# Performance work log

Measured on AMD Instinct MI355X. Metric: run time of the kernel, lower is better.

Reference implementation:

```python
import jax, jax.numpy as jnp
import numpy as np

B, D, N, M, R, C = 512, 16, 64, 32, 32, 10  # batch, divisions, feat_in, feat_map, TR-rank, categories


def setup_inputs() -> dict:
    key = jax.random.key(0)
    k1, k2, k3, k4 = jax.random.split(key, 4)
    tensor = jax.random.normal(k1, (B, D, N), dtype=jnp.float32)
    W_fm = jax.random.normal(k2, (N, M), dtype=jnp.float32) / np.sqrt(N)
    b_fm = jax.random.normal(k3, (M,), dtype=jnp.float32) * 0.01
    # one [R, M, R] tensor-ring core per (category, division)
    G = jax.random.normal(k4, (C, D, R, M, R), dtype=jnp.float32) / np.sqrt(M * R)
    return {"tensor": tensor, "W_fm": W_fm, "b_fm": b_fm, "G": G}


def reference(tensor, W_fm, b_fm, G):
    # FeatureMap: learned linear n -> m applied per division  [B, D, M]
    feat = jnp.einsum('bdn,nm->bdm', tensor, W_fm) + b_fm
    # CoreKernelTensorRing per (category, division): [B,M] x [R,M,R] -> [B,R,R]
    cores = jnp.einsum('bdm,cdimj->cdbij', feat, G)  # [C, D, B, R, R]
    # __foward_products: chained batched matmul along divisions (structural loop, D fixed)
    prod = cores[:, 0]  # [C, B, R, R]
    for d in range(1, D):
        prod = jnp.matmul(prod, cores[:, d])
    # __calculate_traces: per-sample trace, one logit per category
    logits = jnp.einsum('cbii->bc', prod)  # [B, C]
    return jax.nn.log_softmax(logits, axis=1)
```

## Files before the change

### kernel.cpp

```cpp
#include <hip/hip_runtime.h>
#include <math.h>

#define BB 512
#define DD 16
#define NN 64
#define MM 32
#define RR 32
#define CC 10
#define BBLK 8
#define ROWH 40
#define BREGH 1304

typedef _Float16 v8h __attribute__((ext_vector_type(8)));
typedef float v4f __attribute__((ext_vector_type(4)));

union H8 { unsigned int u[4]; v8h h; _Float16 e[8]; };
union H4 { unsigned int u[2]; _Float16 e[4]; };

__global__ __launch_bounds__(256) void produce_kernel(
    const float* __restrict__ tensor, const float* __restrict__ W,
    const float* __restrict__ bias,   const float* __restrict__ G,
    _Float16* __restrict__ fh,        _Float16* __restrict__ gh) {
    __shared__ __align__(16) char smem[36864];
    const int t = threadIdx.x;
    if (blockIdx.x < 1024) {
        float* ten_s = (float*)smem;
        float* W_s   = (float*)smem + 512;
        const int bd0 = blockIdx.x * 8;
        if (t < 128)
            *(float4*)(ten_s + t * 4) = *(const float4*)(tensor + bd0 * NN + t * 4);
        *(float4*)(W_s + t * 4)        = *(const float4*)(W + t * 4);
        *(float4*)(W_s + 1024 + t * 4) = *(const float4*)(W + 1024 + t * 4);
        __syncthreads();
        const int m = t & 31, bd_l = t >> 5;
        float acc = bias[m];
#pragma unroll
        for (int n = 0; n < NN; ++n) acc += ten_s[bd_l * NN + n] * W_s[n * MM + m];
        fh[(bd0 + bd_l) * MM + m] = (_Float16)acc;
    } else {
        _Float16* lg = (_Float16*)smem;
        const int pb = blockIdx.x - 1024;
        const int c  = pb >> 5;
        const int d  = (pb >> 1) & 15;
        const int hf = pb & 1;
        const float* src = G + (size_t)(c * DD + d) * 32768 + hf * 16384;
#pragma unroll
        for (int k = 0; k < 16; ++k) {
            const int f = (k * 256 + t) * 4;
            float4 v = *(const float4*)(src + f);
            const int di = f >> 10, m = (f >> 5) & 31, j = f & 31;
            H4 hv;
            hv.e[0] = (_Float16)v.x; hv.e[1] = (_Float16)v.y;
            hv.e[2] = (_Float16)v.z; hv.e[3] = (_Float16)v.w;
            *(uint2*)(lg + di * 1152 + m * 36 + j) = make_uint2(hv.u[0], hv.u[1]);
        }
        __syncthreads();
#pragma unroll
        for (int k = 0; k < 8; ++k) {
            const int idx = k * 256 + t;
            const int tl = idx >> 6, ln = idx & 63;
            const int di = tl >> 1;
            const int q = ln >> 4, j4 = ln & 15;
            const int j = (tl & 1) * 16 + j4;
            H8 o;
#pragma unroll
            for (int r = 0; r < 8; ++r)
                o.e[r] = lg[di * 1152 + (8 * q + r) * 36 + j];
            const size_t gi = ((size_t)(c * DD + d) * 64 + hf * 32 + tl) * 64 + ln;
            *(v8h*)(gh + gi * 8) = o.h;
        }
    }
}

__global__ __launch_bounds__(512, 4) void chain_kernel(
    const _Float16* __restrict__ feat_h,
    const _Float16* __restrict__ g_h,
    float* __restrict__ logits)
{
    __shared__ __align__(16) _Float16 lds[BBLK * BREGH];

    const int bid = blockIdx.x;
    const int xcd = bid & 7;
    const int idx = bid >> 3;
    int c, sub;
    if (idx < 64) { c = xcd; sub = idx; }
    else {
        const int e = idx - 64;
        if (xcd < 4) { c = 8; sub = xcd * 16 + e; }
        else         { c = 9; sub = (xcd - 4) * 16 + e; }
    }
    const int b0 = sub * BBLK;

    const int t    = threadIdx.x;
    const int w    = t >> 6;
    const int lane = t & 63;
    const int q    = lane >> 4;
    const int j4   = lane & 15;

    const size_t gbase_c = (size_t)c * DD * 32768;
    const int bA = b0 + (j4 & 7);

    v8h afh = *(const v8h*)(feat_h + (size_t)bA * (DD * MM) + q * 8);
    v8h gf[8];
#pragma unroll
    for (int u = 0; u < 8; ++u)
        gf[u] = *(const v8h*)(g_h + gbase_c + ((size_t)(w * 8 + u) * 64 + lane) * 8);

    v8h pah[2];
    v4f acc[2][2];

    for (int d = 0; d < DD; ++d) {
        __syncthreads();
        v4f av[8];
#pragma unroll
        for (int u = 0; u < 8; ++u) {
            v4f z = {0.f, 0.f, 0.f, 0.f};
            av[u] = __builtin_amdgcn_mfma_f32_16x16x32_f16(afh, gf[u], z, 0, 0, 0);
        }
        if (d < DD - 1) {
            afh = *(const v8h*)(feat_h + (size_t)bA * (DD * MM) + (d + 1) * MM + q * 8);
            const size_t gb = gbase_c + (size_t)(d + 1) * 32768;
#pragma unroll
            for (int u = 0; u < 8; ++u)
                gf[u] = *(const v8h*)(g_h + gb + ((size_t)(w * 8 + u) * 64 + lane) * 8);
        }
        if (q < 2) {
#pragma unroll
            for (int jh = 0; jh < 2; ++jh)
#pragma unroll
                for (int reg = 0; reg < 4; ++reg) {
                    H4 hv;
                    hv.e[0] = (_Float16)av[0 + jh][reg];
                    hv.e[1] = (_Float16)av[2 + jh][reg];
                    hv.e[2] = (_Float16)av[4 + jh][reg];
                    hv.e[3] = (_Float16)av[6 + jh][reg];
                    *reinterpret_cast<uint2*>(
                        &lds[(4 * q + reg) * BREGH + (16 * jh + j4) * ROWH + 4 * w]) =
                        make_uint2(hv.u[0], hv.u[1]);
                }
        }
        __syncthreads();
        _Float16* base = lds + w * BREGH;
        if (d == 0) {
#pragma unroll
            for (int mi = 0; mi < 2; ++mi) {
                H8 a;
#pragma unroll
                for (int r = 0; r < 8; ++r)
                    a.e[r] = base[(8 * q + r) * ROWH + 16 * mi + j4];
                pah[mi] = a.h;
            }
        } else {
            v8h bf[2];
#pragma unroll
            for (int ni = 0; ni < 2; ++ni)
                bf[ni] = *(const v8h*)(base + (16 * ni + j4) * ROWH + 8 * q);
#pragma unroll
            for (int mi = 0; mi < 2; ++mi)
#pragma unroll
                for (int ni = 0; ni < 2; ++ni) {
                    v4f z = {0.f, 0.f, 0.f, 0.f};
                    acc[mi][ni] = __builtin_amdgcn_mfma_f32_16x16x32_f16(
                        pah[mi], bf[ni], z, 0, 0, 0);
                }
            if (d < DD - 1) {
#pragma unroll
                for (int mi = 0; mi < 2; ++mi)
#pragma unroll
                    for (int ni = 0; ni < 2; ++ni)
#pragma unroll
                        for (int reg = 0; reg < 4; ++reg)
                            base[(16 * mi + 4 * q + reg) * ROWH + 16 * ni + j4] =
                                (_Float16)acc[mi][ni][reg];
                __builtin_amdgcn_sched_barrier(0);
#pragma unroll
                for (int mi = 0; mi < 2; ++mi)
                    pah[mi] = *(const v8h*)(base + (16 * mi + j4) * ROWH + 8 * q);
            }
        }
    }

    float tr = 0.f;
    if (q == (j4 >> 2)) {
        int reg = j4 & 3;
        tr = acc[0][0][reg] + acc[1][1][reg];
    }
#pragma unroll
    for (int off = 32; off > 0; off >>= 1) tr += __shfl_down(tr, off);
    if (lane == 0) logits[(b0 + w) * CC + c] = tr;
}

__global__ void lsm_kernel(const float* __restrict__ logits,
                           float* __restrict__ out) {
    int b = blockIdx.x * blockDim.x + threadIdx.x;
    if (b >= BB) return;
    float x[CC];
    float mx = -1e30f;
#pragma unroll
    for (int c = 0; c < CC; ++c) { x[c] = logits[b * CC + c]; mx = fmaxf(mx, x[c]); }
    float s = 0.f;
#pragma unroll
    for (int c = 0; c < CC; ++c) s += expf(x[c] - mx);
    float ls = logf(s);
#pragma unroll
    for (int c = 0; c < CC; ++c) out[b * CC + c] = x[c] - mx - ls;
}

extern "C" void kernel_launch(void* const* d_in, const int* in_sizes, int n_in,
                              void* d_out, int out_size, void* d_ws, size_t ws_size,
                              hipStream_t stream) {
    const float* tensor = (const float*)d_in[0];
    const float* W      = (const float*)d_in[1];
    const float* bias   = (const float*)d_in[2];
    const float* G      = (const float*)d_in[3];
    float* out = (float*)d_out;

    const size_t FEAT = (size_t)BB * DD * MM;
    const size_t GPK  = (size_t)CC * DD * 64 * 64 * 8;
    _Float16* fh = (_Float16*)d_ws;
    _Float16* gh = fh + FEAT;
    float* logits = (float*)(gh + GPK);

    produce_kernel<<<1024 + 320, 256, 0, stream>>>(tensor, W, bias, G, fh, gh);
    chain_kernel<<<CC * (BB / BBLK), 512, 0, stream>>>(fh, gh, logits);
    lsm_kernel<<<(BB + 255) / 256, 256, 0, stream>>>(logits, out);
}
```

Before: 124.1 us.

## Halve chain_kernel block to 4 waves, each handling two samples and two tile groups

The chain kernel now launches 256 threads (4 waves) per block instead of 512. Each wave computes two groups of 8 G tiles in the core-construction stage and then runs the serial chain matmul for two batch samples instead of one. The G prefetch for the next division is removed, so G loads now happen inside the loop just before use. This cuts per-block thread count and barrier participants, but it drops the load/compute overlap and doubles the serial per-wave work, so latency per division may grow.

```diff
diff --git a/kernel.cpp b/kernel.cpp
--- a/kernel.cpp
+++ b/kernel.cpp
@@ -72,7 +72,7 @@
     }
 }
 
-__global__ __launch_bounds__(512, 4) void chain_kernel(
+__global__ __launch_bounds__(256, 4) void chain_kernel(
     const _Float16* __restrict__ feat_h,
     const _Float16* __restrict__ g_h,
     float* __restrict__ logits)
@@ -100,94 +100,106 @@
     const size_t gbase_c = (size_t)c * DD * 32768;
     const int bA = b0 + (j4 & 7);
 
-    v8h afh = *(const v8h*)(feat_h + (size_t)bA * (DD * MM) + q * 8);
-    v8h gf[8];
-#pragma unroll
-    for (int u = 0; u < 8; ++u)
-        gf[u] = *(const v8h*)(g_h + gbase_c + ((size_t)(w * 8 + u) * 64 + lane) * 8);
-
-    v8h pah[2];
-    v4f acc[2][2];
+    v8h pah[2][2];
+    v4f acc[2][2][2];
 
     for (int d = 0; d < DD; ++d) {
         __syncthreads();
-        v4f av[8];
-#pragma unroll
-        for (int u = 0; u < 8; ++u) {
-            v4f z = {0.f, 0.f, 0.f, 0.f};
-            av[u] = __builtin_amdgcn_mfma_f32_16x16x32_f16(afh, gf[u], z, 0, 0, 0);
-        }
-        if (d < DD - 1) {
-            afh = *(const v8h*)(feat_h + (size_t)bA * (DD * MM) + (d + 1) * MM + q * 8);
-            const size_t gb = gbase_c + (size_t)(d + 1) * 32768;
-#pragma unroll
-            for (int u = 0; u < 8; ++u)
-                gf[u] = *(const v8h*)(g_h + gb + ((size_t)(w * 8 + u) * 64 + lane) * 8);
-        }
-        if (q < 2) {
-#pragma unroll
-            for (int jh = 0; jh < 2; ++jh)
-#pragma unroll
-                for (int reg = 0; reg < 4; ++reg) {
-                    H4 hv;
-                    hv.e[0] = (_Float16)av[0 + jh][reg];
-                    hv.e[1] = (_Float16)av[2 + jh][reg];
-                    hv.e[2] = (_Float16)av[4 + jh][reg];
-                    hv.e[3] = (_Float16)av[6 + jh][reg];
-                    *reinterpret_cast<uint2*>(
-                        &lds[(4 * q + reg) * BREGH + (16 * jh + j4) * ROWH + 4 * w]) =
-                        make_uint2(hv.u[0], hv.u[1]);
-                }
-        }
-        __syncthreads();
-        _Float16* base = lds + w * BREGH;
-        if (d == 0) {
-#pragma unroll
-            for (int mi = 0; mi < 2; ++mi) {
-                H8 a;
-#pragma unroll
-                for (int r = 0; r < 8; ++r)
-                    a.e[r] = base[(8 * q + r) * ROWH + 16 * mi + j4];
-                pah[mi] = a.h;
+        {
+            const v8h afh = *(const v8h*)(feat_h + (size_t)bA * (DD * MM) + d * MM + q * 8);
+            const size_t gb = gbase_c + (size_t)d * 32768;
+#pragma unroll
+            for (int g = 0; g < 2; ++g) {
+                v8h gf[8];
+#pragma unroll
+                for (int u = 0; u < 8; ++u) {
+                    const int tile = 16 * w + 8 * g + u;
+                    gf[u] = *(const v8h*)(g_h + gb + ((size_t)tile * 64 + lane) * 8);
+                }
+                v4f av[8];
+#pragma unroll
+                for (int u = 0; u < 8; ++u) {
+                    v4f z = {0.f, 0.f, 0.f, 0.f};
+                    av[u] = __builtin_amdgcn_mfma_f32_16x16x32_f16(afh, gf[u], z, 0, 0, 0);
+                }
+                if (q < 2) {
+#pragma unroll
+                    for (int jh = 0; jh < 2; ++jh)
+#pragma unroll
+                        for (int reg = 0; reg < 4; ++reg) {
+                            H4 hv;
+                            hv.e[0] = (_Float16)av[0 + jh][reg];
+                            hv.e[1] = (_Float16)av[2 + jh][reg];
+                            hv.e[2] = (_Float16)av[4 + jh][reg];
+                            hv.e[3] = (_Float16)av[6 + jh][reg];
+                            *reinterpret_cast<uint2*>(
+                                &lds[(4 * q + reg) * BREGH + (16 * jh + j4) * ROWH
+                                     + 8 * w + 4 * g]) = make_uint2(hv.u[0], hv.u[1]);
+                        }
+                }
             }
-        } else {
-            v8h bf[2];
-#pragma unroll
-            for (int ni = 0; ni < 2; ++ni)
-                bf[ni] = *(const v8h*)(base + (16 * ni + j4) * ROWH + 8 * q);
-#pragma unroll
-            for (int mi = 0; mi < 2; ++mi)
-#pragma unroll
-                for (int ni = 0; ni < 2; ++ni) {
-                    v4f z = {0.f, 0.f, 0.f, 0.f};
-                    acc[mi][ni] = __builtin_amdgcn_mfma_f32_16x16x32_f16(
-                        pah[mi], bf[ni], z, 0, 0, 0);
-                }
-            if (d < DD - 1) {
+        }
+        __syncthreads();
+#pragma unroll
+        for (int cc = 0; cc < 2; ++cc) {
+            _Float16* base = lds + (2 * w + cc) * BREGH;
+            if (d == 0) {
+#pragma unroll
+                for (int mi = 0; mi < 2; ++mi) {
+                    H8 a;
+#pragma unroll
+                    for (int r = 0; r < 8; ++r)
+                        a.e[r] = base[(8 * q + r) * ROWH + 16 * mi + j4];
+                    pah[cc][mi] = a.h;
+                }
+            } else {
+                v8h bf[2];
+#pragma unroll
+                for (int ni = 0; ni < 2; ++ni)
+                    bf[ni] = *(const v8h*)(base + (16 * ni + j4) * ROWH + 8 * q);
 #pragma unroll
                 for (int mi = 0; mi < 2; ++mi)
 #pragma unroll
-                    for (int ni = 0; ni < 2; ++ni)
-#pragma unroll
-                        for (int reg = 0; reg < 4; ++reg)
-                            base[(16 * mi + 4 * q + reg) * ROWH + 16 * ni + j4] =
-                                (_Float16)acc[mi][ni][reg];
-                __builtin_amdgcn_sched_barrier(0);
+                    for (int ni = 0; ni < 2; ++ni) {
+                        v4f z = {0.f, 0.f, 0.f, 0.f};
+                        acc[cc][mi][ni] = __builtin_amdgcn_mfma_f32_16x16x32_f16(
+                            pah[cc][mi], bf[ni], z, 0, 0, 0);
+                    }
+                if (d < DD - 1) {
+#pragma unroll
+                    for (int mi = 0; mi < 2; ++mi)
+#pragma unroll
+                        for (int ni = 0; ni < 2; ++ni)
+#pragma unroll
+                            for (int reg = 0; reg < 4; ++reg)
+                                base[(16 * mi + 4 * q + reg) * ROWH + 16 * ni + j4] =
+                                    (_Float16)acc[cc][mi][ni][reg];
+                }
+            }
+        }
+        if (d > 0 && d < DD - 1) {
+            __builtin_amdgcn_sched_barrier(0);
+#pragma unroll
+            for (int cc = 0; cc < 2; ++cc) {
+                _Float16* base = lds + (2 * w + cc) * BREGH;
 #pragma unroll
                 for (int mi = 0; mi < 2; ++mi)
-                    pah[mi] = *(const v8h*)(base + (16 * mi + j4) * ROWH + 8 * q);
+                    pah[cc][mi] = *(const v8h*)(base + (16 * mi + j4) * ROWH + 8 * q);
             }
         }
     }
 
-    float tr = 0.f;
-    if (q == (j4 >> 2)) {
-        int reg = j4 & 3;
-        tr = acc[0][0][reg] + acc[1][1][reg];
-    }
-#pragma unroll
-    for (int off = 32; off > 0; off >>= 1) tr += __shfl_down(tr, off);
-    if (lane == 0) logits[(b0 + w) * CC + c] = tr;
+#pragma unroll
+    for (int cc = 0; cc < 2; ++cc) {
+        float tr = 0.f;
+        if (q == (j4 >> 2)) {
+            int reg = j4 & 3;
+            tr = acc[cc][0][0][reg] + acc[cc][1][1][reg];
+        }
+#pragma unroll
+        for (int off = 32; off > 0; off >>= 1) tr += __shfl_down(tr, off);
+        if (lane == 0) logits[(b0 + 2 * w + cc) * CC + c] = tr;
+    }
 }
 
 __global__ void lsm_kernel(const float* __restrict__ logits,
@@ -222,6 +234,6 @@
     float* logits = (float*)(gh + GPK);
 
     produce_kernel<<<1024 + 320, 256, 0, stream>>>(tensor, W, bias, G, fh, gh);
-    chain_kernel<<<CC * (BB / BBLK), 512, 0, stream>>>(fh, gh, logits);
+    chain_kernel<<<CC * (BB / BBLK), 256, 0, stream>>>(fh, gh, logits);
     lsm_kernel<<<(BB + 255) / 256, 256, 0, stream>>>(logits, out);
 }
```

Result: slower. 127.1 us (+2.5%).
